# Kernel tuning notes

Hardware: AMD Instinct MI355X
Metric: run time of the kernel (lower is better)

The kernel has to match this reference:

```python
import jax, jax.numpy as jnp
import numpy as np

BLOCK = 32          # QLinearLPBQ block_size
W_BITS = 4          # low-precision blockwise weight quantization
ACT_BITS = 16       # ActivationQDQ(bits=16)


def act_qdq(x):
    # per-tensor symmetric 16-bit fake quant-dequant (dynamic absmax scale)
    qmax = 2.0 ** (ACT_BITS - 1) - 1.0  # 32767
    scale = jnp.maximum(jnp.max(jnp.abs(x)) / qmax, 1e-12)
    return jnp.clip(jnp.round(x / scale), -qmax - 1.0, qmax) * scale


def fixed_qdq_u16(x):
    # FixedActivationQDQ: scale = 1/65536, zero_point = 0, unsigned 16-bit grid
    scale = 1.0 / 65536.0
    return jnp.clip(jnp.round(x / scale), 0.0, 65535.0) * scale


def lpbq_dequant(w):
    # blockwise (per output row, per 32-wide input block) 4-bit fake quant-dequant
    O, I = w.shape
    qmax = 2.0 ** (W_BITS - 1) - 1.0  # 7
    wb = w.reshape(O, I // BLOCK, BLOCK)
    s = jnp.maximum(jnp.max(jnp.abs(wb), axis=-1, keepdims=True) / qmax, 1e-12)
    wq = jnp.clip(jnp.round(wb / s), -qmax - 1.0, qmax) * s
    return wq.reshape(O, I)


def setup_inputs() -> dict:
    key = jax.random.key(0)
    k1, k2, k3, k4 = jax.random.split(key, 4)
    B, S, H, I = 2, 4096, 1024, 3072
    x = jax.random.normal(k1, (B, S, H), jnp.float32)
    w_gate = jax.random.normal(k2, (I, H), jnp.float32) * 0.02
    w_up = jax.random.normal(k3, (I, H), jnp.float32) * 0.02
    w_down = jax.random.normal(k4, (H, I), jnp.float32) * 0.02
    return {"x": x, "w_gate": w_gate, "w_up": w_up, "w_down": w_down}


def reference(x, w_gate, w_up, w_down):
    # x: [B, S, H]
    x = act_qdq(x)                                        # up_proj_input_qdq
    up = act_qdq(x @ lpbq_dequant(w_up).T)                # up_proj + output qdq -> [B,S,I]
    gate = act_qdq(x @ lpbq_dequant(w_gate).T)            # gate_proj + output qdq
    sig = fixed_qdq_u16(jax.nn.sigmoid(gate))             # sigmoid on fixed u16 grid
    gate = act_qdq(gate * sig)                            # SiLU (x*sigmoid) + qdq
    o = act_qdq(gate * up)                                # down_proj_input_qdq
    return o @ lpbq_dequant(w_down).T                     # [B, S, H]
```

## Files before the change

### kernel.cpp

```cpp
#include <hip/hip_runtime.h>
#include <hip/hip_bf16.h>
#include <stdint.h>


#define M_ROWS 8192
#define H_DIM 1024
#define I_DIM 3072

typedef unsigned short u16;
typedef unsigned int u32;
typedef __attribute__((ext_vector_type(8))) short bf16x8;
typedef __attribute__((ext_vector_type(4))) float f32x4;

#define WAITVM(n) asm volatile("s_waitcnt vmcnt(" #n ")" ::: "memory")
#define BAR()                                   \
  do {                                          \
    asm volatile("" ::: "memory");              \
    __builtin_amdgcn_s_barrier();               \
    asm volatile("" ::: "memory");              \
  } while (0)

__device__ __forceinline__ float bf2f(u16 v) { return __uint_as_float(((u32)v) << 16); }
__device__ __forceinline__ u16 f2bf(float f) {
  u32 u = __float_as_uint(f);
  u32 r = (u + 0x7fffu + ((u >> 16) & 1u)) >> 16;
  return (u16)r;
}
__device__ __forceinline__ float qdq16i(float x, float inv, float s) {
  float q = rintf(x * inv);
  q = fminf(fmaxf(q, -32768.f), 32767.f);
  return q * s;
}
__device__ __forceinline__ float sigq(float g) {
  float sig = __builtin_amdgcn_rcpf(1.f + __expf(-g));
  return fminf(fmaxf(rintf(sig * 65536.f), 0.f), 65535.f) * (1.f / 65536.f);
}

__device__ __forceinline__ float scale_read(const u32* __restrict__ scal, int s) {
  u32 m = 0;
#pragma unroll
  for (int j = 0; j < 16; ++j) m = max(m, scal[j * 16 + s]);
  return fmaxf(__uint_as_float(m) / 32767.f, 1e-12f);
}

__device__ __forceinline__ void load_lds16(const u16* g, u16* lds) {
  __builtin_amdgcn_global_load_lds(
      (const __attribute__((address_space(1))) u32*)g,
      (__attribute__((address_space(3))) u32*)lds, 16, 0, 0);
}

__device__ __forceinline__ void block_amax_atomic(float mx, u32* scal, int s) {
#pragma unroll
  for (int off = 32; off; off >>= 1) mx = fmaxf(mx, __shfl_xor(mx, off));
  __shared__ float red[4];
  const int lane = threadIdx.x & 63, wave = threadIdx.x >> 6;
  if (lane == 0) red[wave] = mx;
  __syncthreads();
  if (threadIdx.x == 0) {
    float m = fmaxf(fmaxf(red[0], red[1]), fmaxf(red[2], red[3]));
    atomicMax(scal + (blockIdx.x & 15) * 16 + s, __float_as_uint(m));
  }
}

__device__ __forceinline__ void block_amax4(float a, float b, float c, float d,
                                            u32* __restrict__ scal) {
#pragma unroll
  for (int off = 32; off; off >>= 1) {
    a = fmaxf(a, __shfl_xor(a, off));
    b = fmaxf(b, __shfl_xor(b, off));
    c = fmaxf(c, __shfl_xor(c, off));
    d = fmaxf(d, __shfl_xor(d, off));
  }
  __shared__ float red4[4][4];
  const int lane = threadIdx.x & 63, wave = threadIdx.x >> 6;
  if (lane == 0) {
    red4[0][wave] = a;
    red4[1][wave] = b;
    red4[2][wave] = c;
    red4[3][wave] = d;
  }
  __syncthreads();
  if (threadIdx.x == 0) {
    u32* base = scal + (blockIdx.x & 15) * 16;
#pragma unroll
    for (int s = 0; s < 4; ++s) {
      float m = fmaxf(fmaxf(red4[s][0], red4[s][1]), fmaxf(red4[s][2], red4[s][3]));
      atomicMax(base + 1 + s, __float_as_uint(m));
    }
  }
}

__global__ void __launch_bounds__(256, 2) kgemm1(const u16* __restrict__ xq,
                                                 const u16* __restrict__ wcat,
                                                 u16* __restrict__ up, u16* __restrict__ gh,
                                                 u32* __restrict__ scal) {
  __shared__ __align__(16) u16 smem[36864];
  const int tileN = blockIdx.x * 128;
  const int tileM = blockIdx.y * 128;
  const int tid = threadIdx.x;
  const int lane = tid & 63, wave = tid >> 6;
  const int wm = wave >> 1, wn = wave & 1;
  const int quad = lane >> 4, mrow = lane & 15;

  const u16* Ablk = xq + (size_t)tileM * H_DIM;
  const u16* Bublk = wcat + (size_t)tileN * H_DIM;
  const u16* Bgblk = wcat + (size_t)(I_DIM + tileN) * H_DIM;

  int goff[2], loff[2];
#pragma unroll
  for (int t = 0; t < 2; ++t) {
    const int c = tid + 256 * t;
    const int r = c >> 2, q = c & 3;
    goff[t] = r * H_DIM + ((q ^ ((r >> 1) & 3)) << 3);
    loff[t] = c << 3;
  }
  const int pc = (quad ^ ((mrow >> 1) & 3)) << 3;
  int aoff[4], boff[4];
#pragma unroll
  for (int i = 0; i < 4; ++i) {
    aoff[i] = (wm * 64 + i * 16 + mrow) * 32 + pc;
    boff[i] = (wn * 64 + i * 16 + mrow) * 32 + pc;
  }

  f32x4 accg[4][4], accu[4][4];
#pragma unroll
  for (int i = 0; i < 4; ++i)
#pragma unroll
    for (int j = 0; j < 4; ++j) {
      accg[i][j] = (f32x4){0.f, 0.f, 0.f, 0.f};
      accu[i][j] = (f32x4){0.f, 0.f, 0.f, 0.f};
    }

  auto stage = [&](int k0, int bb) {
    u16* d = smem + bb;
#pragma unroll
    for (int t = 0; t < 2; ++t) load_lds16(Ablk + k0 + goff[t], d + loff[t]);
#pragma unroll
    for (int t = 0; t < 2; ++t) load_lds16(Bublk + k0 + goff[t], d + 4096 + loff[t]);
#pragma unroll
    for (int t = 0; t < 2; ++t) load_lds16(Bgblk + k0 + goff[t], d + 8192 + loff[t]);
  };
  auto compute = [&](int bb) {
    const u16* As = smem + bb;
    const u16* Bus = As + 4096;
    const u16* Bgs = As + 8192;
    bf16x8 af[4];
#pragma unroll
    for (int i = 0; i < 4; ++i) af[i] = *(const bf16x8*)&As[aoff[i]];
#pragma unroll
    for (int j = 0; j < 4; ++j) {
      bf16x8 b = *(const bf16x8*)&Bus[boff[j]];
#pragma unroll
      for (int i = 0; i < 4; ++i)
        accu[i][j] = __builtin_amdgcn_mfma_f32_16x16x32_bf16(af[i], b, accu[i][j], 0, 0, 0);
    }
#pragma unroll
    for (int j = 0; j < 4; ++j) {
      bf16x8 b = *(const bf16x8*)&Bgs[boff[j]];
#pragma unroll
      for (int i = 0; i < 4; ++i)
        accg[i][j] = __builtin_amdgcn_mfma_f32_16x16x32_bf16(af[i], b, accg[i][j], 0, 0, 0);
    }
  };

  stage(0, 0);
  stage(32, 12288);
  stage(64, 24576);
  WAITVM(12);
  BAR();

  int bb = 0;
#pragma unroll 1
  for (int t = 0; t < 29; ++t) {
    compute(bb);
    BAR();
    stage((t + 3) * 32, bb);
    WAITVM(12);
    BAR();
    bb = (bb == 24576) ? 0 : bb + 12288;
  }
  compute(bb); BAR(); WAITVM(6); BAR(); bb = (bb == 24576) ? 0 : bb + 12288;
  compute(bb); BAR(); WAITVM(0); BAR(); bb = (bb == 24576) ? 0 : bb + 12288;
  compute(bb);

  const int rb = (lane >> 4) * 4, cb = lane & 15;
  const int erow = lane >> 2, echk = lane & 3;
  u16* gstage = smem + wave * 1152;
  u16* ustage = smem + 12288 + wave * 1152;
  const u16* grb = gstage + erow * 72;
  const u16* urb = ustage + erow * 72;
  float mxg = 0.f, mxu = 0.f, mxh = 0.f, mxo = 0.f;
#pragma unroll
  for (int i = 0; i < 4; ++i) {
    __syncthreads();
#pragma unroll
    for (int j = 0; j < 4; ++j)
#pragma unroll
      for (int r = 0; r < 4; ++r) {
        float g = accg[i][j][r];
        float u = accu[i][j][r];
        mxg = fmaxf(mxg, fabsf(g));
        mxu = fmaxf(mxu, fabsf(u));
        float ha = g * sigq(g);
        mxh = fmaxf(mxh, fabsf(ha));
        mxo = fmaxf(mxo, fabsf(ha * u));
        gstage[(rb + r) * 72 + j * 16 + cb] = f2bf(g);
        ustage[(rb + r) * 72 + j * 16 + cb] = f2bf(u);
      }
    __syncthreads();
    uint4 g0 = *(const uint4*)(grb + echk * 8);
    uint4 g1 = *(const uint4*)(grb + (echk + 4) * 8);
    uint4 u0 = *(const uint4*)(urb + echk * 8);
    uint4 u1 = *(const uint4*)(urb + (echk + 4) * 8);
    size_t grow = (size_t)(tileM + wm * 64 + i * 16 + erow) * I_DIM + (tileN + wn * 64);
    *(uint4*)(gh + grow + echk * 8) = g0;
    *(uint4*)(gh + grow + (echk + 4) * 8) = g1;
    *(uint4*)(up + grow + echk * 8) = u0;
    *(uint4*)(up + grow + (echk + 4) * 8) = u1;
  }
  block_amax4(mxu, mxg, mxh, mxo, scal);
}

__global__ void __launch_bounds__(512, 2) kgemm2(const u16* __restrict__ oq,
                                                 const u16* __restrict__ wdq,
                                                 float* __restrict__ out) {
  __shared__ __align__(16) u16 smem[49152];
  const int tileN = blockIdx.x * 128;
  const int tileM = blockIdx.y * 256;
  const int tid = threadIdx.x;
  const int lane = tid & 63, wave = tid >> 6;
  const int wm = wave >> 1, wn = wave & 1;
  const int quad = lane >> 4, mrow = lane & 15;

  const u16* Ablk = oq + (size_t)tileM * I_DIM;
  const u16* Bblk = wdq + (size_t)tileN * I_DIM;

  int goffA[4], loffA[4], goffB[2], loffB[2];
#pragma unroll
  for (int t = 0; t < 4; ++t) {
    const int c = tid + 512 * t;
    const int r = c >> 3, q = c & 7;
    goffA[t] = r * I_DIM + ((q ^ (r & 7)) << 3);
    loffA[t] = c << 3;
  }
#pragma unroll
  for (int t = 0; t < 2; ++t) {
    const int c = tid + 512 * t;
    const int r = c >> 3, q = c & 7;
    goffB[t] = r * I_DIM + ((q ^ (r & 7)) << 3);
    loffB[t] = c << 3;
  }
  const int pc0 = (quad ^ (mrow & 7)) << 3;
  const int pc1 = ((quad + 4) ^ (mrow & 7)) << 3;
  int arow[4], brow[4];
#pragma unroll
  for (int i = 0; i < 4; ++i) {
    arow[i] = (wm * 64 + i * 16 + mrow) << 6;
    brow[i] = (wn * 64 + i * 16 + mrow) << 6;
  }

  f32x4 acc[4][4];
#pragma unroll
  for (int i = 0; i < 4; ++i)
#pragma unroll
    for (int j = 0; j < 4; ++j) acc[i][j] = (f32x4){0.f, 0.f, 0.f, 0.f};

  {
    u16* d = smem;
#pragma unroll
    for (int t = 0; t < 4; ++t) load_lds16(Ablk + goffA[t], d + loffA[t]);
#pragma unroll
    for (int t = 0; t < 2; ++t) load_lds16(Bblk + goffB[t], d + 16384 + loffB[t]);
  }
  __syncthreads();

  int cur = 0;
  for (int k0 = 0; k0 < I_DIM; k0 += 64) {
    if (k0 + 64 < I_DIM) {
      u16* d = smem + (cur ^ 1) * 24576;
      const int kn = k0 + 64;
#pragma unroll
      for (int t = 0; t < 4; ++t) load_lds16(Ablk + kn + goffA[t], d + loffA[t]);
#pragma unroll
      for (int t = 0; t < 2; ++t) load_lds16(Bblk + kn + goffB[t], d + 16384 + loffB[t]);
    }
    const u16* As = smem + cur * 24576;
    const u16* Bs = As + 16384;
#pragma unroll
    for (int kk = 0; kk < 2; ++kk) {
      const int pc = kk ? pc1 : pc0;
      bf16x8 af[4];
#pragma unroll
      for (int t = 0; t < 4; ++t) af[t] = *(const bf16x8*)&As[arow[t] + pc];
#pragma unroll
      for (int j = 0; j < 4; ++j) {
        bf16x8 b = *(const bf16x8*)&Bs[brow[j] + pc];
#pragma unroll
        for (int i = 0; i < 4; ++i)
          acc[i][j] = __builtin_amdgcn_mfma_f32_16x16x32_bf16(af[i], b, acc[i][j], 0, 0, 0);
      }
    }
    __syncthreads();
    cur ^= 1;
  }

  const int rb = (lane >> 4) * 4, cb = lane & 15;
#pragma unroll
  for (int i = 0; i < 4; ++i) {
#pragma unroll
    for (int j = 0; j < 4; ++j) {
      size_t base = (size_t)(tileM + wm * 64 + i * 16 + rb) * H_DIM +
                    (size_t)(tileN + wn * 64 + j * 16 + cb);
#pragma unroll
      for (int r = 0; r < 4; ++r) out[base + (size_t)r * H_DIM] = acc[i][j][r];
    }
  }
}

__global__ void __launch_bounds__(256) kprep(const float* __restrict__ x,
                                             const float* __restrict__ wu,
                                             const float* __restrict__ wg,
                                             const float* __restrict__ wdn,
                                             u16* __restrict__ wcat, u16* __restrict__ wdq,
                                             u32* __restrict__ scal) {
  if (blockIdx.x < 1024) {
    const float4* x4 = (const float4*)x;
    const int n4 = (M_ROWS * H_DIM) / 4;
    float mx = 0.f;
    for (int i = blockIdx.x * 256 + threadIdx.x; i < n4; i += 1024 * 256) {
      float4 v = x4[i];
      mx = fmaxf(fmaxf(fabsf(v.x), fabsf(v.y)), fmaxf(fmaxf(fabsf(v.z), fabsf(v.w)), mx));
    }
    block_amax_atomic(mx, scal, 0);
    return;
  }
  const int gid = (blockIdx.x - 1024) * 256 + threadIdx.x;
  const int unit = gid >> 3, l8 = gid & 7;
  const float* src;
  u16* dst;
  int u;
  if (unit < 98304)       { src = wu;  dst = wcat;            u = unit; }
  else if (unit < 196608) { src = wg;  dst = wcat + 3145728;  u = unit - 98304; }
  else                    { src = wdn; dst = wdq;             u = unit - 196608; }
  const size_t off = (size_t)u * 32 + (size_t)l8 * 4;
  float4 v = *(const float4*)(src + off);
  float m = fmaxf(fmaxf(fabsf(v.x), fabsf(v.y)), fmaxf(fabsf(v.z), fabsf(v.w)));
  m = fmaxf(m, __shfl_xor(m, 1));
  m = fmaxf(m, __shfl_xor(m, 2));
  m = fmaxf(m, __shfl_xor(m, 4));
  const float s = fmaxf(m / 7.0f, 1e-12f);
  const float inv = 1.0f / s;
  float vv[4] = {v.x, v.y, v.z, v.w};
  u16 o[4];
#pragma unroll
  for (int e = 0; e < 4; ++e) {
    float q = rintf(vv[e] * inv);
    q = fminf(fmaxf(q, -8.f), 7.f);
    o[e] = f2bf(q * s);
  }
  *(ushort4*)(dst + off) = make_ushort4(o[0], o[1], o[2], o[3]);
}

__global__ void __launch_bounds__(256) kqdqx(const float4* __restrict__ x,
                                             ushort4* __restrict__ xq,
                                             const u32* __restrict__ scal) {
  const float s = scale_read(scal, 0);
  const float inv = 1.0f / s;
  const int i = blockIdx.x * 256 + threadIdx.x;
  float4 v = x[i];
  ushort4 o;
  o.x = f2bf(qdq16i(v.x, inv, s));
  o.y = f2bf(qdq16i(v.y, inv, s));
  o.z = f2bf(qdq16i(v.z, inv, s));
  o.w = f2bf(qdq16i(v.w, inv, s));
  xq[i] = o;
}

#define GH4 ((M_ROWS * I_DIM) / 8)
#define EW_BLOCKS 2048

__global__ void __launch_bounds__(256) kmulo(uint4* __restrict__ gh, const uint4* __restrict__ up,
                                             u32* __restrict__ scal) {
  const float sg = scale_read(scal, 2), ig = 1.0f / sg;
  const float sh = scale_read(scal, 3), ih = 1.0f / sh;
  const float su = scale_read(scal, 1), iu = 1.0f / su;
  const float so = scale_read(scal, 4), io = 1.0f / so;
  for (int i = blockIdx.x * 256 + threadIdx.x; i < GH4; i += EW_BLOCKS * 256) {
    union { uint4 v; u16 us[8]; } a, b;
    a.v = gh[i];
    b.v = up[i];
#pragma unroll
    for (int e = 0; e < 8; ++e) {
      float g = qdq16i(bf2f(a.us[e]), ig, sg);
      float h = g * sigq(g);
      float o = qdq16i(h, ih, sh) * qdq16i(bf2f(b.us[e]), iu, su);
      a.us[e] = f2bf(qdq16i(o, io, so));
    }
    gh[i] = a.v;
  }
}

extern "C" void kernel_launch(void* const* d_in, const int* in_sizes, int n_in,
                              void* d_out, int out_size, void* d_ws, size_t ws_size,
                              hipStream_t stream) {
  (void)in_sizes; (void)n_in; (void)out_size; (void)ws_size;
  const float* x   = (const float*)d_in[0];
  const float* wg  = (const float*)d_in[1];
  const float* wu  = (const float*)d_in[2];
  const float* wdn = (const float*)d_in[3];
  float* out = (float*)d_out;
  char* ws = (char*)d_ws;

  u32* scal = (u32*)ws;
  u16* xq   = (u16*)(ws + 1024);
  u16* wcat = xq + (size_t)M_ROWS * H_DIM;
  u16* wdq  = wcat + (size_t)2 * I_DIM * H_DIM;
  u16* up   = wdq + (size_t)H_DIM * I_DIM;
  u16* gh   = up + (size_t)M_ROWS * I_DIM;

  hipMemsetAsync(scal, 0, 1024, stream);
  kprep<<<1024 + 9216, 256, 0, stream>>>(x, wu, wg, wdn, wcat, wdq, scal);
  kqdqx<<<(M_ROWS * H_DIM) / 4 / 256, 256, 0, stream>>>((const float4*)x, (ushort4*)xq, scal);
  kgemm1<<<dim3(24, 64), 256, 0, stream>>>(xq, wcat, up, gh, scal);
  kmulo<<<EW_BLOCKS, 256, 0, stream>>>((uint4*)gh, (const uint4*)up, scal);
  kgemm2<<<dim3(8, 32), 512, 0, stream>>>(gh, wdq, out);
}
```

Baseline: 321.2 us.

## Enlarge gate/up GEMM tile to 256 rows with 4-stage interleaved LDS pipeline

The fused gate/up GEMM now uses 512-thread blocks covering 256x128 output tiles, so each staged B tile of the weights is reused by twice as many A rows. The main loop moves to a 4-buffer LDS ring. The A and B tile loads are split around a mid-iteration barrier so global-to-LDS copies overlap the up and gate MFMA batches, and s_setprio raises priority around the MFMA runs. The tail iterations now issue harmless extra loads past K, and the 128KB of LDS per block limits each CU to one resident block.

```diff
diff --git a/kernel.cpp b/kernel.cpp
--- a/kernel.cpp
+++ b/kernel.cpp
@@ -62,8 +62,8 @@
   }
 }
 
-__device__ __forceinline__ void block_amax4(float a, float b, float c, float d,
-                                            u32* __restrict__ scal) {
+__device__ __forceinline__ void block_amax4_8w(float a, float b, float c, float d,
+                                               u32* __restrict__ scal) {
 #pragma unroll
   for (int off = 32; off; off >>= 1) {
     a = fmaxf(a, __shfl_xor(a, off));
@@ -71,7 +71,7 @@
     c = fmaxf(c, __shfl_xor(c, off));
     d = fmaxf(d, __shfl_xor(d, off));
   }
-  __shared__ float red4[4][4];
+  __shared__ float red4[4][8];
   const int lane = threadIdx.x & 63, wave = threadIdx.x >> 6;
   if (lane == 0) {
     red4[0][wave] = a;
@@ -84,19 +84,21 @@
     u32* base = scal + (blockIdx.x & 15) * 16;
 #pragma unroll
     for (int s = 0; s < 4; ++s) {
-      float m = fmaxf(fmaxf(red4[s][0], red4[s][1]), fmaxf(red4[s][2], red4[s][3]));
+      float m = 0.f;
+#pragma unroll
+      for (int w = 0; w < 8; ++w) m = fmaxf(m, red4[s][w]);
       atomicMax(base + 1 + s, __float_as_uint(m));
     }
   }
 }
 
-__global__ void __launch_bounds__(256, 2) kgemm1(const u16* __restrict__ xq,
+__global__ void __launch_bounds__(512, 2) kgemm1(const u16* __restrict__ xq,
                                                  const u16* __restrict__ wcat,
                                                  u16* __restrict__ up, u16* __restrict__ gh,
                                                  u32* __restrict__ scal) {
-  __shared__ __align__(16) u16 smem[36864];
+  __shared__ __align__(16) u16 smem[65536];
   const int tileN = blockIdx.x * 128;
-  const int tileM = blockIdx.y * 128;
+  const int tileM = blockIdx.y * 256;
   const int tid = threadIdx.x;
   const int lane = tid & 63, wave = tid >> 6;
   const int wm = wave >> 1, wn = wave & 1;
@@ -106,13 +108,20 @@
   const u16* Bublk = wcat + (size_t)tileN * H_DIM;
   const u16* Bgblk = wcat + (size_t)(I_DIM + tileN) * H_DIM;
 
-  int goff[2], loff[2];
+  int goffA[2], loffA[2];
 #pragma unroll
   for (int t = 0; t < 2; ++t) {
-    const int c = tid + 256 * t;
+    const int c = tid + 512 * t;
     const int r = c >> 2, q = c & 3;
-    goff[t] = r * H_DIM + ((q ^ ((r >> 1) & 3)) << 3);
-    loff[t] = c << 3;
+    goffA[t] = r * H_DIM + ((q ^ ((r >> 1) & 3)) << 3);
+    loffA[t] = c << 3;
+  }
+  int goffB, loffB;
+  {
+    const int c = tid;
+    const int r = c >> 2, q = c & 3;
+    goffB = r * H_DIM + ((q ^ ((r >> 1) & 3)) << 3);
+    loffB = c << 3;
   }
   const int pc = (quad ^ ((mrow >> 1) & 3)) << 3;
   int aoff[4], boff[4];
@@ -131,62 +140,60 @@
       accu[i][j] = (f32x4){0.f, 0.f, 0.f, 0.f};
     }
 
-  auto stage = [&](int k0, int bb) {
-    u16* d = smem + bb;
-#pragma unroll
-    for (int t = 0; t < 2; ++t) load_lds16(Ablk + k0 + goff[t], d + loff[t]);
-#pragma unroll
-    for (int t = 0; t < 2; ++t) load_lds16(Bublk + k0 + goff[t], d + 4096 + loff[t]);
-#pragma unroll
-    for (int t = 0; t < 2; ++t) load_lds16(Bgblk + k0 + goff[t], d + 8192 + loff[t]);
+  auto stageA = [&](int k0, u16* d) {
+    load_lds16(Ablk + k0 + goffA[0], d + loffA[0]);
+    load_lds16(Ablk + k0 + goffA[1], d + loffA[1]);
   };
-  auto compute = [&](int bb) {
-    const u16* As = smem + bb;
-    const u16* Bus = As + 4096;
-    const u16* Bgs = As + 8192;
-    bf16x8 af[4];
-#pragma unroll
-    for (int i = 0; i < 4; ++i) af[i] = *(const bf16x8*)&As[aoff[i]];
-#pragma unroll
-    for (int j = 0; j < 4; ++j) {
-      bf16x8 b = *(const bf16x8*)&Bus[boff[j]];
+  auto stageB = [&](int k0, u16* d) {
+    load_lds16(Bublk + k0 + goffB, d + 8192 + loffB);
+    load_lds16(Bgblk + k0 + goffB, d + 12288 + loffB);
+  };
+
+  stageA(0, smem);           stageB(0, smem);
+  stageA(32, smem + 16384);  stageB(32, smem + 16384);
+  stageA(64, smem + 32768);  stageB(64, smem + 32768);
+  WAITVM(8);
+  BAR();
+
+#pragma unroll 1
+  for (int t = 0; t < 32; ++t) {
+    const u16* S = smem + (t & 3) * 16384;
+    u16* D = smem + ((t + 3) & 3) * 16384;
+    const int kn = (t + 3) * 32;
+    bf16x8 af[4], bf[4];
+    stageA(kn, D);
+#pragma unroll
+    for (int i = 0; i < 4; ++i) af[i] = *(const bf16x8*)&S[aoff[i]];
+#pragma unroll
+    for (int j = 0; j < 4; ++j) bf[j] = *(const bf16x8*)&S[8192 + boff[j]];
+    __builtin_amdgcn_s_setprio(1);
+#pragma unroll
+    for (int j = 0; j < 4; ++j)
 #pragma unroll
       for (int i = 0; i < 4; ++i)
-        accu[i][j] = __builtin_amdgcn_mfma_f32_16x16x32_bf16(af[i], b, accu[i][j], 0, 0, 0);
-    }
-#pragma unroll
-    for (int j = 0; j < 4; ++j) {
-      bf16x8 b = *(const bf16x8*)&Bgs[boff[j]];
+        accu[i][j] = __builtin_amdgcn_mfma_f32_16x16x32_bf16(af[i], bf[j], accu[i][j], 0, 0, 0);
+    __builtin_amdgcn_s_setprio(0);
+    BAR();
+    stageB(kn, D);
+#pragma unroll
+    for (int j = 0; j < 4; ++j) bf[j] = *(const bf16x8*)&S[12288 + boff[j]];
+    __builtin_amdgcn_s_setprio(1);
+#pragma unroll
+    for (int j = 0; j < 4; ++j)
 #pragma unroll
       for (int i = 0; i < 4; ++i)
-        accg[i][j] = __builtin_amdgcn_mfma_f32_16x16x32_bf16(af[i], b, accg[i][j], 0, 0, 0);
-    }
-  };
-
-  stage(0, 0);
-  stage(32, 12288);
-  stage(64, 24576);
-  WAITVM(12);
+        accg[i][j] = __builtin_amdgcn_mfma_f32_16x16x32_bf16(af[i], bf[j], accg[i][j], 0, 0, 0);
+    __builtin_amdgcn_s_setprio(0);
+    WAITVM(8);
+    BAR();
+  }
+  WAITVM(0);
   BAR();
-
-  int bb = 0;
-#pragma unroll 1
-  for (int t = 0; t < 29; ++t) {
-    compute(bb);
-    BAR();
-    stage((t + 3) * 32, bb);
-    WAITVM(12);
-    BAR();
-    bb = (bb == 24576) ? 0 : bb + 12288;
-  }
-  compute(bb); BAR(); WAITVM(6); BAR(); bb = (bb == 24576) ? 0 : bb + 12288;
-  compute(bb); BAR(); WAITVM(0); BAR(); bb = (bb == 24576) ? 0 : bb + 12288;
-  compute(bb);
 
   const int rb = (lane >> 4) * 4, cb = lane & 15;
   const int erow = lane >> 2, echk = lane & 3;
   u16* gstage = smem + wave * 1152;
-  u16* ustage = smem + 12288 + wave * 1152;
+  u16* ustage = smem + 16384 + wave * 1152;
   const u16* grb = gstage + erow * 72;
   const u16* urb = ustage + erow * 72;
   float mxg = 0.f, mxu = 0.f, mxh = 0.f, mxo = 0.f;
@@ -218,7 +225,7 @@
     *(uint4*)(up + grow + echk * 8) = u0;
     *(uint4*)(up + grow + (echk + 4) * 8) = u1;
   }
-  block_amax4(mxu, mxg, mxh, mxo, scal);
+  block_amax4_8w(mxu, mxg, mxh, mxo, scal);
 }
 
 __global__ void __launch_bounds__(512, 2) kgemm2(const u16* __restrict__ oq,
@@ -421,7 +428,7 @@
   hipMemsetAsync(scal, 0, 1024, stream);
   kprep<<<1024 + 9216, 256, 0, stream>>>(x, wu, wg, wdn, wcat, wdq, scal);
   kqdqx<<<(M_ROWS * H_DIM) / 4 / 256, 256, 0, stream>>>((const float4*)x, (ushort4*)xq, scal);
-  kgemm1<<<dim3(24, 64), 256, 0, stream>>>(xq, wcat, up, gh, scal);
+  kgemm1<<<dim3(24, 32), 512, 0, stream>>>(xq, wcat, up, gh, scal);
   kmulo<<<EW_BLOCKS, 256, 0, stream>>>((uint4*)gh, (const uint4*)up, scal);
   kgemm2<<<dim3(8, 32), 512, 0, stream>>>(gh, wdq, out);
 }
```

After: 338.3 us. 1.05x slower.
